# Performance work log

Measured on AMD Instinct MI355X. Metric: run time of the kernel, lower is better.

Reference implementation:

```python
import jax, jax.numpy as jnp
import numpy as np

E, H, F, N, B = 512, 8, 2048, 1024, 4
HD = E // H


def setup_inputs() -> dict:
    key = jax.random.key(0)
    ks = jax.random.split(key, 20)
    s = 0.02
    return {
        "node_inputs": jax.random.normal(ks[0], (N, B, E), jnp.float32),
        "parent_mask": jax.random.uniform(ks[1], (B, N, N), jnp.float32),
        "hidden": jax.random.bernoulli(ks[2], 0.5, (B, N, N)),
        "pad_mask": jax.random.bernoulli(ks[3], 0.1, (B, N)),
        "Wp": jax.random.normal(ks[4], (H, E), jnp.float32) * s,
        "bp": jnp.zeros((H,), jnp.float32),
        "Wc": jax.random.normal(ks[5], (H, E), jnp.float32) * s,
        "bc": jnp.zeros((H,), jnp.float32),
        "Wqkv": jax.random.normal(ks[6], (3 * E, E), jnp.float32) * s,
        "bqkv": jnp.zeros((3 * E,), jnp.float32),
        "Wo": jax.random.normal(ks[7], (E, E), jnp.float32) * s,
        "bo": jnp.zeros((E,), jnp.float32),
        "W1": jax.random.normal(ks[8], (F, E), jnp.float32) * s,
        "b1": jnp.zeros((F,), jnp.float32),
        "W2": jax.random.normal(ks[9], (E, F), jnp.float32) * s,
        "b2": jnp.zeros((E,), jnp.float32),
        "ln1_g": jnp.ones((E,), jnp.float32),
        "ln1_b": jnp.zeros((E,), jnp.float32),
        "ln2_g": jnp.ones((E,), jnp.float32),
        "ln2_b": jnp.zeros((E,), jnp.float32),
    }


def _layer_norm(x, g, b, eps=1e-5):
    m = jnp.mean(x, axis=-1, keepdims=True)
    v = jnp.mean((x - m) ** 2, axis=-1, keepdims=True)
    return (x - m) * jax.lax.rsqrt(v + eps) * g + b


def reference(node_inputs, parent_mask, hidden, pad_mask, Wp, bp, Wc, bc,
              Wqkv, bqkv, Wo, bo, W1, b1, W2, b2, ln1_g, ln1_b, ln2_g, ln2_b):
    x = node_inputs  # (N, B, E), seq-first like nn.TransformerEncoderLayer
    # parent/child per-head biases: Linear(E->H), permuted to (B, H, N)
    pbias = jnp.transpose(x @ Wp.T + bp, (1, 2, 0))
    cbias = jnp.transpose(x @ Wc.T + bc, (1, 2, 0))
    # additive attention bias (B, H, N, N)
    am = (jnp.swapaxes(parent_mask, 1, 2)[:, None] * pbias[..., None]
          + parent_mask[:, None] * cbias[..., None])
    am = jnp.where(hidden[:, None], -jnp.inf, am)
    # multi-head self-attention
    qkv = x @ Wqkv.T + bqkv  # (N, B, 3E)
    q, k, v = jnp.split(qkv, 3, axis=-1)

    def heads(t):  # (N, B, E) -> (B, H, N, HD)
        return jnp.transpose(t.reshape(N, B, H, HD), (1, 2, 0, 3))

    q, k, v = heads(q), heads(k), heads(v)
    scores = jnp.einsum("bhqd,bhkd->bhqk", q, k) / jnp.sqrt(jnp.float32(HD)) + am
    scores = jnp.where(pad_mask[:, None, None, :], -jnp.inf, scores)
    attn = jax.nn.softmax(scores, axis=-1)
    ctx = jnp.einsum("bhqk,bhkd->bhqd", attn, v)  # (B, H, N, HD)
    ctx = jnp.transpose(ctx, (2, 0, 1, 3)).reshape(N, B, E)
    attn_out = ctx @ Wo.T + bo
    # post-norm transformer encoder layer (dropout=0, relu activation)
    y = _layer_norm(x + attn_out, ln1_g, ln1_b)
    ff = jax.nn.relu(y @ W1.T + b1) @ W2.T + b2
    return _layer_norm(y + ff, ln2_g, ln2_b)
```

## Files before the change

### kernel.cpp

```cpp
#include <hip/hip_runtime.h>
#include <hip/hip_bf16.h>
#include <stdint.h>

using bf16 = __hip_bfloat16;

typedef __bf16 bf16x8 __attribute__((ext_vector_type(8)));
typedef float  f32x4  __attribute__((ext_vector_type(4)));

__device__ __forceinline__ float bflo(uint32_t u) { return __uint_as_float(u << 16); }
__device__ __forceinline__ float bfhi(uint32_t u) { return __uint_as_float(u & 0xffff0000u); }

__device__ __forceinline__ void load8(const bf16* p, float* f) {
  uint4 u = *(const uint4*)p;
  f[0] = bflo(u.x); f[1] = bfhi(u.x);
  f[2] = bflo(u.y); f[3] = bfhi(u.y);
  f[4] = bflo(u.z); f[5] = bfhi(u.z);
  f[6] = bflo(u.w); f[7] = bfhi(u.w);
}
__device__ __forceinline__ void load8(const float* p, float* f) {
  float4 a = *(const float4*)p, b = *(const float4*)(p + 4);
  f[0] = a.x; f[1] = a.y; f[2] = a.z; f[3] = a.w;
  f[4] = b.x; f[5] = b.y; f[6] = b.z; f[7] = b.w;
}
__device__ __forceinline__ void store1(float* o, float v) { *o = v; }
__device__ __forceinline__ void store1(bf16* o, float v) { *o = __float2bfloat16(v); }
__device__ __forceinline__ uint32_t bfbits(float x) {
  bf16 v = __float2bfloat16(x);
  return (uint32_t)*(uint16_t*)&v;
}

typedef const uint32_t __attribute__((address_space(1)))* gp_t;
typedef uint32_t __attribute__((address_space(3)))* lp_t;
__device__ __forceinline__ void gload16(const void* g, void* l) {
  __builtin_amdgcn_global_load_lds((gp_t)g, (lp_t)l, 16, 0, 0);
}

__global__ __launch_bounds__(256)
void cvt_prep(const float* __restrict__ x, const float* __restrict__ Wqkv,
              const float* __restrict__ Wo, const float* __restrict__ W1,
              const float* __restrict__ W2, bf16* __restrict__ xb,
              bf16* __restrict__ wq, bf16* __restrict__ wob,
              bf16* __restrict__ w1b, bf16* __restrict__ w2b,
              const float* __restrict__ bqkv, const float* __restrict__ bp,
              const float* __restrict__ bc, const float* __restrict__ Wp,
              const float* __restrict__ Wc, float* __restrict__ bias_ext)
{
  const int blk = blockIdx.x, t = threadIdx.x;
  if (blk < 2560) {
    size_t j = ((size_t)blk * 256 + t) * 8;
    const float* s; bf16* o; size_t off;
    if      (j < 2097152) { s = x;    o = xb;  off = j; }
    else if (j < 2883584) { s = Wqkv; o = wq;  off = j - 2097152; }
    else if (j < 3145728) { s = Wo;   o = wob; off = j - 2883584; }
    else if (j < 4194304) { s = W1;   o = w1b; off = j - 3145728; }
    else                  { s = W2;   o = w2b; off = j - 4194304; }
    float f[8];
    load8(s + off, f);
    uint4 u;
    u.x = (bfbits(f[1]) << 16) | bfbits(f[0]);
    u.y = (bfbits(f[3]) << 16) | bfbits(f[2]);
    u.z = (bfbits(f[5]) << 16) | bfbits(f[4]);
    u.w = (bfbits(f[7]) << 16) | bfbits(f[6]);
    *(uint4*)(o + off) = u;
  } else {
    int sb = blk - 2560;
    if (sb < 2) {
      int j = (sb * 256 + t) * 8;
      if (j < 4096) {
        float f[8]; load8(Wp + j, f);
#pragma unroll
        for (int i = 0; i < 8; ++i) wq[(size_t)1536 * 512 + j + i] = __float2bfloat16(f[i]);
      }
    } else if (sb < 4) {
      int j = ((sb - 2) * 256 + t) * 8;
      if (j < 4096) {
        float f[8]; load8(Wc + j, f);
#pragma unroll
        for (int i = 0; i < 8; ++i) wq[(size_t)1544 * 512 + j + i] = __float2bfloat16(f[i]);
      }
    } else {
      int j = t * 8;
#pragma unroll
      for (int i = 0; i < 8; ++i) {
        int cc = j + i;
        if (cc < 1664) {
          float v = 0.f;
          if (cc < 1536) v = bqkv[cc];
          else if (cc < 1544) v = bp[cc - 1536];
          else if (cc < 1552) v = bc[cc - 1544];
          bias_ext[cc] = v;
        }
      }
    }
  }
}

__global__ __launch_bounds__(256)
void qkv_mask(const bf16* __restrict__ A, const bf16* __restrict__ W,
              const float* __restrict__ bias, bf16* __restrict__ outb,
              float* __restrict__ outf,
              const float* __restrict__ pm, const int* __restrict__ hid,
              const int* __restrict__ padm, uint32_t* __restrict__ mout)
{
  __shared__ char smem[33280];
  const int blk = blockIdx.x, t = threadIdx.x;
  if (blk < 416) {
    bf16* As = (bf16*)smem;
    bf16* Bs = (bf16*)(smem + 16384);
    const int lane = t & 63, wave = t >> 6;
    const int m0 = (blk / 13) * 128, n0 = (blk % 13) * 128;
    const int wr = wave >> 1, wc = wave & 1;
    const int frow = lane & 15, ksel = (lane >> 4) * 8;
    f32x4 acc[16] = {};
    const bf16* Ab = A + (size_t)m0 * 512;
    const bf16* Wb = W + (size_t)n0 * 512;
    for (int k0 = 0; k0 < 512; k0 += 64) {
      __syncthreads();
#pragma unroll
      for (int i = 0; i < 4; ++i) {
        int ib = i * 256 + wave * 64;
        int idx = ib + lane;
        gload16(Ab + (size_t)(idx >> 3) * 512 + k0 + (idx & 7) * 8, As + ib * 8);
      }
#pragma unroll
      for (int i = 0; i < 4; ++i) {
        int ib = i * 256 + wave * 64;
        int idx = ib + lane;
        gload16(Wb + (size_t)(idx >> 3) * 512 + k0 + (idx & 7) * 8, Bs + ib * 8);
      }
      __syncthreads();
#pragma unroll
      for (int kk = 0; kk < 64; kk += 32) {
        bf16x8 af[4], bf_[4];
#pragma unroll
        for (int mt = 0; mt < 4; ++mt)
          af[mt] = *(const bf16x8*)(As + (wr * 64 + mt * 16 + frow) * 64 + kk + ksel);
#pragma unroll
        for (int nt = 0; nt < 4; ++nt)
          bf_[nt] = *(const bf16x8*)(Bs + (wc * 64 + nt * 16 + frow) * 64 + kk + ksel);
#pragma unroll
        for (int mt = 0; mt < 4; ++mt)
#pragma unroll
          for (int nt = 0; nt < 4; ++nt)
            acc[mt * 4 + nt] = __builtin_amdgcn_mfma_f32_16x16x32_bf16(
                af[mt], bf_[nt], acc[mt * 4 + nt], 0, 0, 0);
      }
    }
    const int rb = (lane >> 4) * 4, cb = lane & 15;
#pragma unroll
    for (int mt = 0; mt < 4; ++mt)
#pragma unroll
      for (int nt = 0; nt < 4; ++nt) {
        f32x4 a = acc[mt * 4 + nt];
#pragma unroll
        for (int r = 0; r < 4; ++r) {
          int row = m0 + wr * 64 + mt * 16 + rb + r;
          int col = n0 + wc * 64 + nt * 16 + cb;
          if (col >= 1552) continue;
          float v = a[r] + bias[col];
          int n = row >> 2, b = row & 3;
          if (col >= 1536) {
            int j = col - 1536;
            int hh = j & 7;
            outf[(j < 8 ? 0 : 32768) + (b * 8 + hh) * 1024 + n] = v;
          } else {
            int which = col >> 9, hh = (col >> 6) & 7, d = col & 63;
            if (which == 0) v *= 0.125f;
            size_t idx;
            if (which == 2)
              idx = (((size_t)(64 + b * 8 + hh)) << 16) + (size_t)d * 1024 + n;
            else
              idx = (((size_t)(which * 32 + b * 8 + hh)) << 16) + (size_t)n * 64 + d;
            outb[idx] = __float2bfloat16(v);
          }
        }
      }
  } else {
    float (*tileT)[65] = (float(*)[65])smem;
    const int mb = blk - 416;
    const int k0 = (mb & 7) * 128, q0 = ((mb >> 3) & 15) * 64, b = mb >> 7;
    const size_t pb = (size_t)b << 20;
#pragma unroll
    for (int i = 0; i < 32; ++i) {
      int idx = t + i * 256;
      int r = idx >> 6, c = idx & 63;
      tileT[r][c] = pm[pb + (size_t)(k0 + r) * 1024 + q0 + c];
    }
    __syncthreads();
#pragma unroll
    for (int i = 0; i < 32; ++i) {
      int idx = t + i * 256;
      int q = idx >> 7, k = idx & 127;
      size_t src = pb + (size_t)(q0 + q) * 1024 + k0 + k;
      int msk = hid[src] | padm[b * 1024 + k0 + k];
      uint32_t u = 0xFFFFFFFFu;
      if (!msk) u = (bfbits(tileT[k][q]) << 16) | bfbits(pm[src]);
      mout[src] = u;
    }
  }
}

template<int MODE, int BN>
__global__ __launch_bounds__(256)
void gemm_bt(const bf16* __restrict__ A, const bf16* __restrict__ W,
             const float* __restrict__ bias, bf16* __restrict__ outb,
             float* __restrict__ outf, int M, int Nout, int K, int kLen)
{
  constexpr int NT = BN / 32;
  __shared__ bf16 As[128 * 64];
  __shared__ bf16 Bs[BN * 64];
  const int t = threadIdx.x, lane = t & 63, wave = t >> 6;
  const int m0 = blockIdx.y * 128, n0 = blockIdx.x * BN;
  const int kOff = blockIdx.z * kLen;
  if (MODE == 3) outf += (size_t)blockIdx.z * M * Nout;
  const int wr = wave >> 1, wc = wave & 1;
  const int frow = lane & 15, ksel = (lane >> 4) * 8;
  f32x4 acc[4 * NT] = {};
  const bf16* Ab = A + (size_t)m0 * K;
  const bf16* Wb = W + (size_t)n0 * K;

  for (int k0 = kOff; k0 < kOff + kLen; k0 += 64) {
    __syncthreads();
#pragma unroll
    for (int i = 0; i < 4; ++i) {
      int ib = i * 256 + wave * 64;
      int idx = ib + lane;
      gload16(Ab + (size_t)(idx >> 3) * K + k0 + (idx & 7) * 8, As + ib * 8);
    }
#pragma unroll
    for (int i = 0; i < BN / 32; ++i) {
      int ib = i * 256 + wave * 64;
      int idx = ib + lane;
      gload16(Wb + (size_t)(idx >> 3) * K + k0 + (idx & 7) * 8, Bs + ib * 8);
    }
    __syncthreads();
#pragma unroll
    for (int kk = 0; kk < 64; kk += 32) {
      bf16x8 af[4], bf_[NT];
#pragma unroll
      for (int mt = 0; mt < 4; ++mt)
        af[mt] = *(const bf16x8*)(As + (wr * 64 + mt * 16 + frow) * 64 + kk + ksel);
#pragma unroll
      for (int nt = 0; nt < NT; ++nt)
        bf_[nt] = *(const bf16x8*)(Bs + (wc * (BN / 2) + nt * 16 + frow) * 64 + kk + ksel);
#pragma unroll
      for (int mt = 0; mt < 4; ++mt)
#pragma unroll
        for (int nt = 0; nt < NT; ++nt)
          acc[mt * NT + nt] = __builtin_amdgcn_mfma_f32_16x16x32_bf16(
              af[mt], bf_[nt], acc[mt * NT + nt], 0, 0, 0);
    }
  }
  const int rb = (lane >> 4) * 4, cb = lane & 15;
#pragma unroll
  for (int mt = 0; mt < 4; ++mt)
#pragma unroll
    for (int nt = 0; nt < NT; ++nt) {
      f32x4 a = acc[mt * NT + nt];
#pragma unroll
      for (int r = 0; r < 4; ++r) {
        int row = m0 + wr * 64 + mt * 16 + rb + r;
        int col = n0 + wc * (BN / 2) + nt * 16 + cb;
        if (MODE == 3) {
          outf[(size_t)row * Nout + col] = a[r];
        } else {
          float v = a[r] + bias[col];
          if (MODE == 1) v = fmaxf(v, 0.f);
          outb[(size_t)row * Nout + col] = __float2bfloat16(v);
        }
      }
    }
}

__global__ __launch_bounds__(256, 3)
void attn_mfma(const bf16* __restrict__ qkv, const float* __restrict__ pbw,
               const float* __restrict__ cbw, const uint32_t* __restrict__ mpk,
               bf16* __restrict__ opart, float2* __restrict__ mlout)
{
  __shared__ bf16 Kt[128 * 64];
  __shared__ bf16 Vt[64 * 128];
  __shared__ bf16 Ps[4][16][136];
  const int t = threadIdx.x, lane = t & 63, wave = t >> 6;
  const int g = lane >> 4, c = lane & 15;
  const int h = blockIdx.y, b = blockIdx.z >> 1, half = blockIdx.z & 1;
  const int q0 = blockIdx.x * 64 + wave * 16;
  const size_t bh = (size_t)b * 8 + h;
  const bf16* Qp = qkv + (bh << 16);
  const bf16* Kp = qkv + ((32 + bh) << 16);
  const bf16* Vg = qkv + ((64 + bh) << 16);

  bf16x8 qa0 = *(const bf16x8*)(Qp + (size_t)(q0 + c) * 64 + g * 8);
  bf16x8 qa1 = *(const bf16x8*)(Qp + (size_t)(q0 + c) * 64 + 32 + g * 8);

  const float pbq = pbw[bh * 1024 + q0 + c];
  const float cbq = cbw[bh * 1024 + q0 + c];
  const uint32_t* mrp = mpk + (((size_t)b * 1024 + q0 + c) << 10);

  f32x4 oacc[4] = {{0,0,0,0},{0,0,0,0},{0,0,0,0},{0,0,0,0}};
  float m = -1e30f, l = 0.f;

  for (int kt = 0; kt < 4; ++kt) {
    const int k0 = half * 512 + kt * 128;
    __syncthreads();
#pragma unroll
    for (int i = 0; i < 4; ++i) {
      int ib = i * 256 + wave * 64;
      int idx = ib + lane;
      int r = idx >> 3, p = idx & 7;
      gload16(Kp + (size_t)(k0 + r) * 64 + ((p ^ (r & 7)) * 8), Kt + ib * 8);
    }
#pragma unroll
    for (int i = 0; i < 4; ++i) {
      int ib = i * 256 + wave * 64;
      int idx = ib + lane;
      int d = idx >> 4, p = idx & 15;
      gload16(Vg + (size_t)d * 1024 + k0 + ((p ^ (d & 15)) * 8), Vt + ib * 8);
    }
    uint4 mu[8];
#pragma unroll
    for (int nt = 0; nt < 8; ++nt)
      mu[nt] = *(const uint4*)(mrp + k0 + nt * 16 + 4 * g);
    __syncthreads();
    f32x4 sacc[8];
#pragma unroll
    for (int nt = 0; nt < 8; ++nt) {
      f32x4 z = {0.f,0.f,0.f,0.f};
      int r = nt * 16 + c;
      bf16x8 k0f = *(const bf16x8*)(Kt + r * 64 + (( g      ^ (c & 7)) * 8));
      bf16x8 k1f = *(const bf16x8*)(Kt + r * 64 + (((4 + g) ^ (c & 7)) * 8));
      z = __builtin_amdgcn_mfma_f32_16x16x32_bf16(k0f, qa0, z, 0, 0, 0);
      z = __builtin_amdgcn_mfma_f32_16x16x32_bf16(k1f, qa1, z, 0, 0, 0);
      sacc[nt] = z;
    }
    float mx = -1e30f;
#pragma unroll
    for (int nt = 0; nt < 8; ++nt) {
      uint32_t uu[4] = {mu[nt].x, mu[nt].y, mu[nt].z, mu[nt].w};
#pragma unroll
      for (int r = 0; r < 4; ++r) {
        float s = sacc[nt][r] + bfhi(uu[r]) * pbq + bflo(uu[r]) * cbq;
        s = (uu[r] == 0xFFFFFFFFu) ? -1e30f : s;
        sacc[nt][r] = s;
        mx = fmaxf(mx, s);
      }
    }
    mx = fmaxf(mx, __shfl_xor(mx, 16));
    mx = fmaxf(mx, __shfl_xor(mx, 32));
    const float newm = fmaxf(m, mx);
    const float al = __expf(m - newm);
    float ps = 0.f;
#pragma unroll
    for (int nt = 0; nt < 8; ++nt) {
      float p0 = (sacc[nt][0] <= -1e29f) ? 0.f : __expf(sacc[nt][0] - newm);
      float p1 = (sacc[nt][1] <= -1e29f) ? 0.f : __expf(sacc[nt][1] - newm);
      float p2 = (sacc[nt][2] <= -1e29f) ? 0.f : __expf(sacc[nt][2] - newm);
      float p3 = (sacc[nt][3] <= -1e29f) ? 0.f : __expf(sacc[nt][3] - newm);
      ps += (p0 + p1) + (p2 + p3);
      uint2 w;
      w.x = (bfbits(p1) << 16) | bfbits(p0);
      w.y = (bfbits(p3) << 16) | bfbits(p2);
      *(uint2*)&Ps[wave][c][nt * 16 + 4 * g] = w;
    }
    ps += __shfl_xor(ps, 16);
    ps += __shfl_xor(ps, 32);
    l = l * al + ps;
    m = newm;
#pragma unroll
    for (int dt = 0; dt < 4; ++dt) {
      oacc[dt][0] *= al; oacc[dt][1] *= al;
      oacc[dt][2] *= al; oacc[dt][3] *= al;
    }
#pragma unroll
    for (int dt = 0; dt < 4; ++dt) {
      int row = dt * 16 + c;
#pragma unroll
      for (int kc = 0; kc < 4; ++kc) {
        bf16x8 vf = *(const bf16x8*)(Vt + row * 128 + (((kc * 4 + g) ^ c) * 8));
        bf16x8 pf = *(const bf16x8*)&Ps[wave][c][kc * 32 + g * 8];
        oacc[dt] = __builtin_amdgcn_mfma_f32_16x16x32_bf16(vf, pf, oacc[dt], 0, 0, 0);
      }
    }
  }
  const int qg = q0 + c;
  const size_t prow = ((size_t)(half * 32) + bh) * 1024 + qg;
#pragma unroll
  for (int dt = 0; dt < 4; ++dt)
#pragma unroll
    for (int rg = 0; rg < 4; ++rg)
      opart[prow * 64 + dt * 16 + 4 * g + rg] = __float2bfloat16(oacc[dt][rg]);
  if (g == 0) mlout[prow] = make_float2(m, l);
}

__global__ __launch_bounds__(256)
void attn_reduce(const bf16* __restrict__ opart, const float2* __restrict__ ml,
                 bf16* __restrict__ ctxo)
{
  const int idx = blockIdx.x * 256 + threadIdx.x;
  const int row = idx >> 3, seg = (idx & 7) * 8;
  float o0[8], o1[8];
  load8(opart + (size_t)row * 64 + seg, o0);
  load8(opart + (size_t)(row + 32768) * 64 + seg, o1);
  const float2 ml0 = ml[row], ml1 = ml[row + 32768];
  const float mst = fmaxf(ml0.x, ml1.x);
  const float w0 = __expf(ml0.x - mst), w1 = __expf(ml1.x - mst);
  const float denom = ml0.y * w0 + ml1.y * w1;
  const float inv = (denom > 0.f) ? 1.f / denom : 0.f;
  const int bh = row >> 10, q = row & 1023;
  const int b = bh >> 3, h = bh & 7;
  bf16* out = ctxo + ((size_t)q * 4 + b) * 512 + h * 64 + seg;
#pragma unroll
  for (int j = 0; j < 8; ++j)
    out[j] = __float2bfloat16((o0[j] * w0 + o1[j] * w1) * inv);
}

template<typename TA, typename TO>
__global__ __launch_bounds__(256)
void ln_res2(const TA* __restrict__ a, const float* __restrict__ p0,
             const float* __restrict__ p1, const float* __restrict__ bias,
             const float* __restrict__ g, const float* __restrict__ be,
             TO* __restrict__ out)
{
  const int wave = threadIdx.x >> 6, lane = threadIdx.x & 63;
  const int m = blockIdx.x * 4 + wave;
  const size_t base = (size_t)m * 512 + lane * 8;
  float va[8], f0[8], f1[8], bb[8];
  load8(a + base, va);
  load8(p0 + base, f0);
  load8(p1 + base, f1);
  load8(bias + lane * 8, bb);
  float v[8], s = 0.f;
#pragma unroll
  for (int j = 0; j < 8; ++j) { v[j] = va[j] + f0[j] + f1[j] + bb[j]; s += v[j]; }
#pragma unroll
  for (int off = 32; off; off >>= 1) s += __shfl_xor(s, off);
  const float mean = s * (1.f / 512.f);
  float q = 0.f;
#pragma unroll
  for (int j = 0; j < 8; ++j) { float d = v[j] - mean; q += d * d; }
#pragma unroll
  for (int off = 32; off; off >>= 1) q += __shfl_xor(q, off);
  const float rs = rsqrtf(q * (1.f / 512.f) + 1e-5f);
  float gv[8], bv[8];
  load8(g + lane * 8, gv);
  load8(be + lane * 8, bv);
#pragma unroll
  for (int j = 0; j < 8; ++j)
    store1(out + base + j, (v[j] - mean) * rs * gv[j] + bv[j]);
}

extern "C" void kernel_launch(void* const* d_in, const int* in_sizes, int n_in,
                              void* d_out, int out_size, void* d_ws, size_t ws_size,
                              hipStream_t stream)
{
  (void)in_sizes; (void)n_in; (void)out_size; (void)ws_size;
  const float* x    = (const float*)d_in[0];
  const float* pm   = (const float*)d_in[1];
  const int*   hid  = (const int*)d_in[2];
  const int*   padm = (const int*)d_in[3];
  const float* Wp   = (const float*)d_in[4];
  const float* bp   = (const float*)d_in[5];
  const float* Wc   = (const float*)d_in[6];
  const float* bc   = (const float*)d_in[7];
  const float* Wqkv = (const float*)d_in[8];
  const float* bqkv = (const float*)d_in[9];
  const float* Wo   = (const float*)d_in[10];
  const float* bo   = (const float*)d_in[11];
  const float* W1   = (const float*)d_in[12];
  const float* b1   = (const float*)d_in[13];
  const float* W2   = (const float*)d_in[14];
  const float* b2   = (const float*)d_in[15];
  const float* g1   = (const float*)d_in[16];
  const float* be1  = (const float*)d_in[17];
  const float* g2   = (const float*)d_in[18];
  const float* be2  = (const float*)d_in[19];

  char* ws = (char*)d_ws;
  bf16*     qkvb  = (bf16*)    (ws);
  float*    pbo   = (float*)   (ws + 12582912);
  float*    cbo   = (float*)   (ws + 12713984);
  uint32_t* mpk   = (uint32_t*)(ws + 12845056);
  bf16*     ctx   = (bf16*)    (ws + 29622272);
  float*    part  = (float*)   (ws);
  bf16*     ff1   = (bf16*)    (ws + 16777216);
  bf16*     y     = (bf16*)    (ws + 33816576);
  bf16*     xb    = (bf16*)    (ws + 38010880);
  bf16*     wqkvb = (bf16*)    (ws + 42205184);
  bf16*     wob   = (bf16*)    (ws + 43909120);
  bf16*     w1b   = (bf16*)    (ws + 44433408);
  bf16*     w2b   = (bf16*)    (ws + 46530560);
  float*    bext  = (float*)   (ws + 48627712);
  bf16*     opart = (bf16*)    (ws + 48634368);
  float2*   mlb   = (float2*)  (ws + 57022976);
  float*    part1 = part + (size_t)4096 * 512;

  cvt_prep<<<2565, 256, 0, stream>>>(x, Wqkv, Wo, W1, W2, xb, wqkvb, wob, w1b, w2b,
                                     bqkv, bp, bc, Wp, Wc, bext);
  qkv_mask<<<928, 256, 0, stream>>>(xb, wqkvb, bext, qkvb, pbo,
                                    pm, hid, padm, mpk);
  attn_mfma<<<dim3(16, 8, 8), 256, 0, stream>>>(qkvb, pbo, cbo, mpk, opart, mlb);
  attn_reduce<<<1024, 256, 0, stream>>>(opart, mlb, ctx);
  gemm_bt<3, 64><<<dim3(8, 32, 2), 256, 0, stream>>>(ctx, wob, nullptr, nullptr, part, 4096, 512, 512, 256);
  ln_res2<float, bf16><<<1024, 256, 0, stream>>>(x, part, part1, bo, g1, be1, y);
  gemm_bt<1, 128><<<dim3(16, 32), 256, 0, stream>>>(y, w1b, b1, ff1, nullptr, 4096, 2048, 512, 512);
  gemm_bt<3, 64><<<dim3(8, 32, 2), 256, 0, stream>>>(ff1, w2b, nullptr, nullptr, part, 4096, 512, 2048, 1024);
  ln_res2<bf16, float><<<1024, 256, 0, stream>>>(y, part, part1, b2, g2, be2, (float*)d_out);
}
```

Before: 267.7 us.

## Split fused QKV/mask kernel and double-buffer QKV GEMM shared-memory tiles

Splits the combined QKV-projection and mask-packing kernel into two separate launches: a standalone mask_pack kernel and a qkv_gemm kernel. The GEMM now double-buffers its A/B tiles in LDS (64 KB), issuing the next k-slice's loads before computing the current one, with one barrier per iteration. This is meant to hide global-load latency behind the MFMA work. In exchange it adds a kernel launch, loses the overlap of the mask work with the GEMM blocks, and the larger LDS footprint may lower occupancy.

```diff
diff --git a/kernel.cpp b/kernel.cpp
--- a/kernel.cpp
+++ b/kernel.cpp
@@ -96,108 +96,120 @@
 }
 
 __global__ __launch_bounds__(256)
-void qkv_mask(const bf16* __restrict__ A, const bf16* __restrict__ W,
+void mask_pack(const float* __restrict__ pm, const int* __restrict__ hid,
+               const int* __restrict__ padm, uint32_t* __restrict__ mout)
+{
+  __shared__ float tileT[128][65];
+  const int t = threadIdx.x, mb = blockIdx.x;
+  const int k0 = (mb & 7) * 128, q0 = ((mb >> 3) & 15) * 64, b = mb >> 7;
+  const size_t pb = (size_t)b << 20;
+#pragma unroll
+  for (int i = 0; i < 32; ++i) {
+    int idx = t + i * 256;
+    int r = idx >> 6, c = idx & 63;
+    tileT[r][c] = pm[pb + (size_t)(k0 + r) * 1024 + q0 + c];
+  }
+  __syncthreads();
+#pragma unroll
+  for (int i = 0; i < 32; ++i) {
+    int idx = t + i * 256;
+    int q = idx >> 7, k = idx & 127;
+    size_t src = pb + (size_t)(q0 + q) * 1024 + k0 + k;
+    int msk = hid[src] | padm[b * 1024 + k0 + k];
+    uint32_t u = 0xFFFFFFFFu;
+    if (!msk) u = (bfbits(tileT[k][q]) << 16) | bfbits(pm[src]);
+    mout[src] = u;
+  }
+}
+
+__global__ __launch_bounds__(256)
+void qkv_gemm(const bf16* __restrict__ A, const bf16* __restrict__ W,
               const float* __restrict__ bias, bf16* __restrict__ outb,
-              float* __restrict__ outf,
-              const float* __restrict__ pm, const int* __restrict__ hid,
-              const int* __restrict__ padm, uint32_t* __restrict__ mout)
-{
-  __shared__ char smem[33280];
-  const int blk = blockIdx.x, t = threadIdx.x;
-  if (blk < 416) {
-    bf16* As = (bf16*)smem;
-    bf16* Bs = (bf16*)(smem + 16384);
-    const int lane = t & 63, wave = t >> 6;
-    const int m0 = (blk / 13) * 128, n0 = (blk % 13) * 128;
-    const int wr = wave >> 1, wc = wave & 1;
-    const int frow = lane & 15, ksel = (lane >> 4) * 8;
-    f32x4 acc[16] = {};
-    const bf16* Ab = A + (size_t)m0 * 512;
-    const bf16* Wb = W + (size_t)n0 * 512;
-    for (int k0 = 0; k0 < 512; k0 += 64) {
-      __syncthreads();
-#pragma unroll
-      for (int i = 0; i < 4; ++i) {
-        int ib = i * 256 + wave * 64;
-        int idx = ib + lane;
-        gload16(Ab + (size_t)(idx >> 3) * 512 + k0 + (idx & 7) * 8, As + ib * 8);
-      }
-#pragma unroll
-      for (int i = 0; i < 4; ++i) {
-        int ib = i * 256 + wave * 64;
-        int idx = ib + lane;
-        gload16(Wb + (size_t)(idx >> 3) * 512 + k0 + (idx & 7) * 8, Bs + ib * 8);
-      }
-      __syncthreads();
-#pragma unroll
-      for (int kk = 0; kk < 64; kk += 32) {
-        bf16x8 af[4], bf_[4];
-#pragma unroll
-        for (int mt = 0; mt < 4; ++mt)
-          af[mt] = *(const bf16x8*)(As + (wr * 64 + mt * 16 + frow) * 64 + kk + ksel);
+              float* __restrict__ outf)
+{
+  __shared__ bf16 As[2][128 * 64];
+  __shared__ bf16 Bs[2][128 * 64];
+  const int t = threadIdx.x;
+  const int lane = t & 63, wave = t >> 6;
+  const int m0 = (blockIdx.x / 13) * 128, n0 = (blockIdx.x % 13) * 128;
+  const int wr = wave >> 1, wc = wave & 1;
+  const int frow = lane & 15, ksel = (lane >> 4) * 8;
+  f32x4 acc[16] = {};
+  const bf16* Ab = A + (size_t)m0 * 512;
+  const bf16* Wb = W + (size_t)n0 * 512;
+
+  const int ibs = wave * 64 + lane;
+#define STAGE(buf, k0)                                                        \
+  {                                                                           \
+    _Pragma("unroll")                                                         \
+    for (int i = 0; i < 4; ++i) {                                             \
+      int idx = i * 256 + ibs;                                                \
+      gload16(Ab + (size_t)(idx >> 3) * 512 + (k0) + (idx & 7) * 8,           \
+              &As[buf][(i * 256 + wave * 64) * 8]);                           \
+    }                                                                         \
+    _Pragma("unroll")                                                         \
+    for (int i = 0; i < 4; ++i) {                                             \
+      int idx = i * 256 + ibs;                                                \
+      gload16(Wb + (size_t)(idx >> 3) * 512 + (k0) + (idx & 7) * 8,           \
+              &Bs[buf][(i * 256 + wave * 64) * 8]);                           \
+    }                                                                         \
+  }
+
+  STAGE(0, 0);
+  __syncthreads();
+#pragma unroll
+  for (int ks = 0; ks < 8; ++ks) {
+    const int cur = ks & 1;
+    if (ks < 7) STAGE(cur ^ 1, (ks + 1) * 64);
+#pragma unroll
+    for (int kk = 0; kk < 64; kk += 32) {
+      bf16x8 af[4], bf_[4];
+#pragma unroll
+      for (int mt = 0; mt < 4; ++mt)
+        af[mt] = *(const bf16x8*)(&As[cur][(wr * 64 + mt * 16 + frow) * 64 + kk + ksel]);
+#pragma unroll
+      for (int nt = 0; nt < 4; ++nt)
+        bf_[nt] = *(const bf16x8*)(&Bs[cur][(wc * 64 + nt * 16 + frow) * 64 + kk + ksel]);
+#pragma unroll
+      for (int mt = 0; mt < 4; ++mt)
 #pragma unroll
         for (int nt = 0; nt < 4; ++nt)
-          bf_[nt] = *(const bf16x8*)(Bs + (wc * 64 + nt * 16 + frow) * 64 + kk + ksel);
-#pragma unroll
-        for (int mt = 0; mt < 4; ++mt)
-#pragma unroll
-          for (int nt = 0; nt < 4; ++nt)
-            acc[mt * 4 + nt] = __builtin_amdgcn_mfma_f32_16x16x32_bf16(
-                af[mt], bf_[nt], acc[mt * 4 + nt], 0, 0, 0);
-      }
-    }
-    const int rb = (lane >> 4) * 4, cb = lane & 15;
-#pragma unroll
-    for (int mt = 0; mt < 4; ++mt)
-#pragma unroll
-      for (int nt = 0; nt < 4; ++nt) {
-        f32x4 a = acc[mt * 4 + nt];
-#pragma unroll
-        for (int r = 0; r < 4; ++r) {
-          int row = m0 + wr * 64 + mt * 16 + rb + r;
-          int col = n0 + wc * 64 + nt * 16 + cb;
-          if (col >= 1552) continue;
-          float v = a[r] + bias[col];
-          int n = row >> 2, b = row & 3;
-          if (col >= 1536) {
-            int j = col - 1536;
-            int hh = j & 7;
-            outf[(j < 8 ? 0 : 32768) + (b * 8 + hh) * 1024 + n] = v;
-          } else {
-            int which = col >> 9, hh = (col >> 6) & 7, d = col & 63;
-            if (which == 0) v *= 0.125f;
-            size_t idx;
-            if (which == 2)
-              idx = (((size_t)(64 + b * 8 + hh)) << 16) + (size_t)d * 1024 + n;
-            else
-              idx = (((size_t)(which * 32 + b * 8 + hh)) << 16) + (size_t)n * 64 + d;
-            outb[idx] = __float2bfloat16(v);
-          }
+          acc[mt * 4 + nt] = __builtin_amdgcn_mfma_f32_16x16x32_bf16(
+              af[mt], bf_[nt], acc[mt * 4 + nt], 0, 0, 0);
+    }
+    __syncthreads();
+  }
+#undef STAGE
+
+  const int rb = (lane >> 4) * 4, cb = lane & 15;
+#pragma unroll
+  for (int mt = 0; mt < 4; ++mt)
+#pragma unroll
+    for (int nt = 0; nt < 4; ++nt) {
+      f32x4 a = acc[mt * 4 + nt];
+#pragma unroll
+      for (int r = 0; r < 4; ++r) {
+        int row = m0 + wr * 64 + mt * 16 + rb + r;
+        int col = n0 + wc * 64 + nt * 16 + cb;
+        if (col >= 1552) continue;
+        float v = a[r] + bias[col];
+        int n = row >> 2, b = row & 3;
+        if (col >= 1536) {
+          int j = col - 1536;
+          int hh = j & 7;
+          outf[(j < 8 ? 0 : 32768) + (b * 8 + hh) * 1024 + n] = v;
+        } else {
+          int which = col >> 9, hh = (col >> 6) & 7, d = col & 63;
+          if (which == 0) v *= 0.125f;
+          size_t idx;
+          if (which == 2)
+            idx = (((size_t)(64 + b * 8 + hh)) << 16) + (size_t)d * 1024 + n;
+          else
+            idx = (((size_t)(which * 32 + b * 8 + hh)) << 16) + (size_t)n * 64 + d;
+          outb[idx] = __float2bfloat16(v);
         }
       }
-  } else {
-    float (*tileT)[65] = (float(*)[65])smem;
-    const int mb = blk - 416;
-    const int k0 = (mb & 7) * 128, q0 = ((mb >> 3) & 15) * 64, b = mb >> 7;
-    const size_t pb = (size_t)b << 20;
-#pragma unroll
-    for (int i = 0; i < 32; ++i) {
-      int idx = t + i * 256;
-      int r = idx >> 6, c = idx & 63;
-      tileT[r][c] = pm[pb + (size_t)(k0 + r) * 1024 + q0 + c];
-    }
-    __syncthreads();
-#pragma unroll
-    for (int i = 0; i < 32; ++i) {
-      int idx = t + i * 256;
-      int q = idx >> 7, k = idx & 127;
-      size_t src = pb + (size_t)(q0 + q) * 1024 + k0 + k;
-      int msk = hid[src] | padm[b * 1024 + k0 + k];
-      uint32_t u = 0xFFFFFFFFu;
-      if (!msk) u = (bfbits(tileT[k][q]) << 16) | bfbits(pm[src]);
-      mout[src] = u;
-    }
-  }
+    }
 }
 
 template<int MODE, int BN>
@@ -495,8 +507,8 @@
 
   cvt_prep<<<2565, 256, 0, stream>>>(x, Wqkv, Wo, W1, W2, xb, wqkvb, wob, w1b, w2b,
                                      bqkv, bp, bc, Wp, Wc, bext);
-  qkv_mask<<<928, 256, 0, stream>>>(xb, wqkvb, bext, qkvb, pbo,
-                                    pm, hid, padm, mpk);
+  mask_pack<<<512, 256, 0, stream>>>(pm, hid, padm, mpk);
+  qkv_gemm<<<416, 256, 0, stream>>>(xb, wqkvb, bext, qkvb, pbo);
   attn_mfma<<<dim3(16, 8, 8), 256, 0, stream>>>(qkvb, pbo, cbo, mpk, opart, mlb);
   attn_reduce<<<1024, 256, 0, stream>>>(opart, mlb, ctx);
   gemm_bt<3, 64><<<dim3(8, 32, 2), 256, 0, stream>>>(ctx, wob, nullptr, nullptr, part, 4096, 512, 512, 256);
```

Result: slower. 276.0 us (+3.1%).
